# Performance work log

Hardware: AMD Instinct MI355X
Metric: run time of the kernel (lower is better)

The kernel has to match this reference:

```python
import jax, jax.numpy as jnp
import numpy as np
import math

B, S, D = 4, 2048, 1024
TAU = 0.5

def setup_inputs() -> dict:
    key = jax.random.key(0)
    ks = jax.random.split(key, 10)
    s = 1.0 / math.sqrt(D)
    return {
        "node_emb": jax.random.normal(ks[0], (B, S, D), jnp.float32),
        "label_emb": jax.random.normal(ks[1], (B, S, D), jnp.float32),
        "Wq": jax.random.uniform(ks[2], (D, D), jnp.float32, -s, s),
        "bq": jax.random.uniform(ks[3], (D,), jnp.float32, -s, s),
        "Wk": jax.random.uniform(ks[4], (D, D), jnp.float32, -s, s),
        "bk": jax.random.uniform(ks[5], (D,), jnp.float32, -s, s),
        "Wv": jax.random.uniform(ks[6], (D, D), jnp.float32, -s, s),
        "bv": jax.random.uniform(ks[7], (D,), jnp.float32, -s, s),
        "Wp": jax.random.uniform(ks[8], (D, D), jnp.float32, -s, s),
        "bp": jax.random.uniform(ks[9], (D,), jnp.float32, -s, s),
    }

def reference(node_emb, label_emb, Wq, bq, Wk, bk, Wv, bv, Wp, bp):
    # Q from label_emb; K, V from node_emb (torch Linear: x @ W.T + b)
    Q = label_emb @ Wq.T + bq          # [B, S, D]
    K = node_emb @ Wk.T + bk           # [B, S, D]
    V = node_emb @ Wv.T + bv           # [B, S, D]
    d = node_emb.shape[-1]
    score = jnp.einsum('bqd,bkd->bqk', Q, K) / jnp.sqrt(jnp.float32(d))
    # causal (lower-triangular) mask, masked_fill(-1e9) BEFORE the tau scale
    causal = jnp.tril(jnp.ones((score.shape[-2], score.shape[-1]), bool))
    score = jnp.where(causal[None, :, :], score, jnp.float32(-1e9))
    attn = jax.nn.softmax(score * TAU, axis=-1)  # [B, S, S]
    # proj_drop is Dropout(0.1); reference runs in eval mode (identity)
    z = jnp.einsum('bqk,bkd->bqd', attn, V)
    return z @ Wp.T + bp
```

## Files before the change

### kernel.cpp

```cpp
#include <hip/hip_runtime.h>
#include <hip/hip_bf16.h>
#include <stdint.h>

using bf16 = __hip_bfloat16;
typedef __bf16 bf16x8 __attribute__((ext_vector_type(8)));
typedef float f32x4 __attribute__((ext_vector_type(4)));
typedef unsigned short u16x8 __attribute__((ext_vector_type(8)));
typedef unsigned short u16x4 __attribute__((ext_vector_type(4)));

#define AS1 __attribute__((address_space(1)))
#define AS3 __attribute__((address_space(3)))

__device__ inline unsigned short f2b(float f) {
    union { __hip_bfloat16 h; unsigned short u; } cv;
    cv.h = __float2bfloat16(f);
    return cv.u;
}

__global__ __launch_bounds__(256) void cvt6(
    const float* __restrict__ i0, const float* __restrict__ i1,
    const float* __restrict__ i2, const float* __restrict__ i3,
    const float* __restrict__ i4, const float* __restrict__ i5,
    u16x8* __restrict__ o0, u16x8* __restrict__ o1,
    u16x8* __restrict__ o2, u16x8* __restrict__ o3,
    u16x8* __restrict__ o4, u16x8* __restrict__ o5,
    long nbig, long nsmall)
{
    const int y = blockIdx.y;
    const float* in = y == 0 ? i0 : (y == 1 ? i1 : (y == 2 ? i2 : (y == 3 ? i3 : (y == 4 ? i4 : i5))));
    u16x8* out = y == 0 ? o0 : (y == 1 ? o1 : (y == 2 ? o2 : (y == 3 ? o3 : (y == 4 ? o4 : o5))));
    const long n8 = (y < 2) ? nbig : nsmall;
    long i = (long)blockIdx.x * blockDim.x + threadIdx.x;
    const long stride = (long)gridDim.x * blockDim.x;
    const float4* in4 = (const float4*)in;
    for (; i < n8; i += stride) {
        float4 x = in4[2 * i], z = in4[2 * i + 1];
        u16x8 o;
        o[0] = f2b(x.x); o[1] = f2b(x.y); o[2] = f2b(x.z); o[3] = f2b(x.w);
        o[4] = f2b(z.x); o[5] = f2b(z.y); o[6] = f2b(z.z); o[7] = f2b(z.w);
        out[i] = o;
    }
}

template <typename T> __device__ inline void storev(T* p, float v);
template <> __device__ inline void storev<float>(float* p, float v) { *p = v; }
template <> __device__ inline void storev<bf16>(bf16* p, float v) { *p = __float2bfloat16(v); }

template <typename OutT, int MODE, int BN>
__global__ __launch_bounds__(512, 2) void gemmX(
    const bf16* __restrict__ A0, const bf16* __restrict__ A1,
    const bf16* __restrict__ B0p, const bf16* __restrict__ B1p,
    OutT* __restrict__ C0, OutT* __restrict__ C1,
    const float* __restrict__ bias0, const float* __restrict__ bias1,
    float scale, int lda, int ldb, int ldc, int Kdim,
    long sA, long sB, long sC)
{
    constexpr int LDSZ = (BN == 256) ? 131072 : ((MODE == 3) ? 99328 : 98304);
    constexpr int BUFS = (BN == 256) ? 65536 : 49152;
    __shared__ __align__(16) char lds[LDSZ];

    const int nwg = gridDim.x;
    const int bid = blockIdx.x;
    const int s = (nwg & 7) ? bid : ((bid & 7) * (nwg >> 3) + (bid >> 3));

    int bm, ccol0, rowB0, seg = 0, bn_s = 0, zidx = 0;
    const bf16 *A, *B;
    OutT* C;
    const float* bias = nullptr;

    if constexpr (MODE == 0) {
        bm = s >> 3; const int bnl = s & 7; seg = bnl >> 2;
        A = A0; B = B0p; rowB0 = bnl * 256;
        C = seg ? C1 : C0; bias = seg ? bias1 : bias0;
        ccol0 = (bnl & 3) * 256;
    } else if constexpr (MODE == 1) {
        seg = s >> 7; const int r = s & 127; bm = r >> 2; const int bn = r & 3;
        A = seg ? A1 : A0; B = seg ? B1p : B0p;
        C = seg ? C1 : C0; bias = seg ? nullptr : bias0;
        rowB0 = bn * 256; ccol0 = bn * 256;
    } else if constexpr (MODE == 2) {
        const int z = s / 36, f = s % 36;
        int m = 0;
        while ((m + 1) * (m + 2) / 2 <= f) ++m;
        bm = m; const int bn = f - m * (m + 1) / 2;
        bn_s = bn; zidx = z;
        A = A0 + (long)z * sA; B = B0p + (long)z * sB; C = C0 + (long)z * sC;
        rowB0 = bn * 256; ccol0 = bn * 256;
    } else {
        const int z = s >> 6, r = s & 63; bm = r >> 3; const int bn = r & 7;
        zidx = z;
        A = A0 + (long)z * sA; B = B0p + (long)z * sB; C = C0 + (long)z * sC;
        rowB0 = bn * 128; ccol0 = bn * 128; bias = bias0;
    }

    int KT = Kdim >> 6;
    if constexpr (MODE == 3) { const int lim = 4 * (bm + 1); if (lim < KT) KT = lim; }
    const int NIT = KT >> 1;

    const int tid = threadIdx.x;
    const int lane = tid & 63;
    const int w = tid >> 6;
    constexpr int WR = (BN == 256) ? 128 : 64;
    const int wm = (BN == 256) ? (w >> 2) : (w >> 1);
    const int wn = (BN == 256) ? (w & 3) : (w & 1);

    const int rowA0 = bm * 256;

    float* invl = (float*)(lds + 98304);
    if constexpr (MODE == 3) {
        if (tid < 256) {
            const float* part = (const float*)B1p + (((long)zidx * 8 + bm) * 32) * 256 + tid;
            float sum = 0.f;
            const int n4 = 4 * (bm + 1);
            for (int b4 = 0; b4 < n4; ++b4) sum += part[(long)b4 * 256];
            invl[tid] = 1.0f / sum;
        }
        asm volatile("s_waitcnt lgkmcnt(0)" ::: "memory");
        __builtin_amdgcn_sched_barrier(0);
    }

    const int rr  = tid >> 3;
    const int lch = (tid & 7) ^ (rr & 7);
    const bf16* gAt = A + (long)(rowA0 + rr) * lda + lch * 8;
    const bf16* gBt = B + (long)(rowB0 + rr) * ldb + lch * 8;

#define LA(b) (lds + (b) * BUFS)
#define LB(b) (lds + 32768 + (b) * BUFS)

    auto SG2 = [&](const bf16* g, int ld, char* dst) {
        __builtin_amdgcn_global_load_lds((const AS1 void*)g,
            (AS3 void*)(dst + tid * 16), 16, 0, 0);
        __builtin_amdgcn_global_load_lds((const AS1 void*)(g + (long)64 * ld),
            (AS3 void*)(dst + 8192 + tid * 16), 16, 0, 0);
    };
    auto ST_A = [&](int kt, int half, int b) {
        SG2(gAt + (long)kt * 64 + (long)half * 128 * lda, lda, LA(b) + half * 16384);
    };
    auto ST_B = [&](int kt, int half, int b) {
        SG2(gBt + (long)kt * 64 + (long)half * 128 * ldb, ldb, LB(b) + half * 16384);
    };
    auto ST_B1 = [&](int kt, int b) {
        SG2(gBt + (long)kt * 64, ldb, LB(b));
    };

    const int abase = (wm * WR + (lane & 15)) * 128;
    const int bbase = (wn * 64 + (lane & 15)) * 128;
    const int cc0 = (((lane >> 4) << 4)) ^ ((lane & 7) << 4);
    const int cc1 = cc0 ^ 64;

#define RAF(b, mh, mi, kk) (*(const bf16x8*)(LA(b) + abase + (mh)*8192 + (mi)*2048 + ((kk) ? cc1 : cc0)))
#define RBF(b, ni, kk)     (*(const bf16x8*)(LB(b) + bbase + (ni)*2048 + ((kk) ? cc1 : cc0)))

    f32x4 acc[(BN == 256) ? 8 : 4][4] = {};
    bf16x8 ar[4][2], blo[2][2], bhi[2][2];

#define RD_A2(b, mh, MI0) { ar[MI0][0] = RAF(b, mh, MI0, 0); ar[MI0][1] = RAF(b, mh, MI0, 1); \
                            ar[(MI0)+1][0] = RAF(b, mh, (MI0)+1, 0); ar[(MI0)+1][1] = RAF(b, mh, (MI0)+1, 1); }
#define RD_BLO(b)   { blo[0][0] = RBF(b, 0, 0); blo[0][1] = RBF(b, 0, 1); blo[1][0] = RBF(b, 1, 0); blo[1][1] = RBF(b, 1, 1); }
#define RD_BHI(b)   { bhi[0][0] = RBF(b, 2, 0); bhi[0][1] = RBF(b, 2, 1); bhi[1][0] = RBF(b, 3, 0); bhi[1][1] = RBF(b, 3, 1); }

#define MQ1(MI, bb, MH, NB) { \
    f32x4 t0_ = acc[(MH)*4 + (MI)][(NB)]; \
    t0_ = __builtin_amdgcn_mfma_f32_16x16x32_bf16(ar[MI][0], bb[0][0], t0_, 0, 0, 0); \
    t0_ = __builtin_amdgcn_mfma_f32_16x16x32_bf16(ar[MI][1], bb[0][1], t0_, 0, 0, 0); \
    acc[(MH)*4 + (MI)][(NB)] = t0_; \
    f32x4 t1_ = acc[(MH)*4 + (MI)][(NB) + 1]; \
    t1_ = __builtin_amdgcn_mfma_f32_16x16x32_bf16(ar[MI][0], bb[1][0], t1_, 0, 0, 0); \
    t1_ = __builtin_amdgcn_mfma_f32_16x16x32_bf16(ar[MI][1], bb[1][1], t1_, 0, 0, 0); \
    acc[(MH)*4 + (MI)][(NB) + 1] = t1_; }

#define WAIT_LGKM0 { asm volatile("s_waitcnt lgkmcnt(0)" ::: "memory"); __builtin_amdgcn_sched_barrier(0); }
#define WAIT_LGKM4 { asm volatile("s_waitcnt lgkmcnt(4)" ::: "memory"); __builtin_amdgcn_sched_barrier(0); }
#define SCHEDB     __builtin_amdgcn_sched_barrier(0)
#define PRE_SYNC { asm volatile("s_waitcnt lgkmcnt(0)" ::: "memory"); __builtin_amdgcn_sched_barrier(0); \
                   __builtin_amdgcn_s_barrier(); __builtin_amdgcn_sched_barrier(0); }

    auto BAR = [&]() { __builtin_amdgcn_s_barrier(); SCHEDB; };
    auto PRIO1 = [&]() { __builtin_amdgcn_s_setprio(1); };
    auto PRIO0 = [&]() { __builtin_amdgcn_s_setprio(0); };

    if constexpr (BN == 256) {
        ST_A(0, 0, 0); ST_A(0, 1, 0); ST_B(0, 0, 0); ST_B(0, 1, 0);
        ST_B(1, 0, 1); ST_B(1, 1, 1);
        asm volatile("s_waitcnt vmcnt(4)" ::: "memory");
        BAR();
        RD_BLO(0); RD_A2(0, 0, 0); RD_A2(0, 0, 2);

        for (int i = 0; i < NIT; ++i) {
            const int t0 = 2 * i;
            const bool last = (i == NIT - 1);

            ST_A(t0 + 1, 0, 1);
            PRE_SYNC; PRIO1();
            RD_BHI(0);
            MQ1(0, blo, 0, 0); MQ1(1, blo, 0, 0); MQ1(2, blo, 0, 0); MQ1(3, blo, 0, 0);
            PRIO0();

            ST_A(t0 + 1, 1, 1);
            PRE_SYNC; PRIO1();
            MQ1(0, bhi, 0, 2); MQ1(1, bhi, 0, 2); MQ1(2, bhi, 0, 2); MQ1(3, bhi, 0, 2);
            RD_A2(0, 1, 0); RD_A2(0, 1, 2);
            PRIO0();

            if (!last) ST_B(t0 + 2, 0, 0);
            PRE_SYNC; PRIO1();
            MQ1(0, bhi, 1, 2); MQ1(1, bhi, 1, 2); MQ1(2, bhi, 1, 2); MQ1(3, bhi, 1, 2);
            PRIO0();

            if (!last) { ST_B(t0 + 2, 1, 0);
                         asm volatile("s_waitcnt vmcnt(4)" ::: "memory"); }
            else       { asm volatile("s_waitcnt vmcnt(0)" ::: "memory"); }
            PRE_SYNC; PRIO1();
            MQ1(0, blo, 1, 0); MQ1(1, blo, 1, 0); MQ1(2, blo, 1, 0); MQ1(3, blo, 1, 0);
            RD_BLO(1); RD_A2(1, 0, 0); RD_A2(1, 0, 2);
            PRIO0();

            if (!last) ST_A(t0 + 2, 0, 0);
            PRE_SYNC; PRIO1();
            RD_BHI(1);
            MQ1(0, blo, 0, 0); MQ1(1, blo, 0, 0); MQ1(2, blo, 0, 0); MQ1(3, blo, 0, 0);
            PRIO0();

            if (!last) ST_A(t0 + 2, 1, 0);
            PRE_SYNC; PRIO1();
            MQ1(0, bhi, 0, 2); MQ1(1, bhi, 0, 2); MQ1(2, bhi, 0, 2); MQ1(3, bhi, 0, 2);
            RD_A2(1, 1, 0); RD_A2(1, 1, 2);
            PRIO0();

            if (!last) ST_B(t0 + 3, 0, 1);
            PRE_SYNC; PRIO1();
            MQ1(0, bhi, 1, 2); MQ1(1, bhi, 1, 2); MQ1(2, bhi, 1, 2); MQ1(3, bhi, 1, 2);
            PRIO0();

            if (!last) { ST_B(t0 + 3, 1, 1);
                         asm volatile("s_waitcnt vmcnt(4)" ::: "memory"); }
            PRE_SYNC; PRIO1();
            MQ1(0, blo, 1, 0); MQ1(1, blo, 1, 0); MQ1(2, blo, 1, 0); MQ1(3, blo, 1, 0);
            if (!last) { RD_BLO(0); RD_A2(0, 0, 0); RD_A2(0, 0, 2); }
            PRIO0();
        }
    } else {
        ST_A(0, 0, 0); ST_A(0, 1, 0); ST_B1(0, 0);
        ST_A(1, 0, 1); ST_A(1, 1, 1); ST_B1(1, 1);
        asm volatile("s_waitcnt vmcnt(6)" ::: "memory");
        BAR();

        for (int i = 0; i < NIT; ++i) {
            const int t0 = 2 * i;
            const bool last = (i == NIT - 1);

            RD_BLO(0); RD_A2(0, 0, 0); RD_A2(0, 0, 2); SCHEDB; RD_BHI(0);
            BAR(); WAIT_LGKM4; PRIO1();
            MQ1(0, blo, 0, 0); MQ1(1, blo, 0, 0); MQ1(2, blo, 0, 0); MQ1(3, blo, 0, 0);
            PRIO0(); BAR();

            if (!last) { ST_A(t0 + 2, 0, 0); ST_A(t0 + 2, 1, 0);
                         asm volatile("s_waitcnt vmcnt(4)" ::: "memory"); }
            else       { asm volatile("s_waitcnt vmcnt(0)" ::: "memory"); }
            BAR(); WAIT_LGKM0; PRIO1();
            MQ1(0, bhi, 0, 2); MQ1(1, bhi, 0, 2); MQ1(2, bhi, 0, 2); MQ1(3, bhi, 0, 2);
            PRIO0(); BAR();

            RD_BLO(1); RD_A2(1, 0, 0); RD_A2(1, 0, 2); SCHEDB; RD_BHI(1);
            if (!last) ST_B1(t0 + 2, 0);
            BAR(); WAIT_LGKM4; PRIO1();
            MQ1(0, blo, 0, 0); MQ1(1, blo, 0, 0); MQ1(2, blo, 0, 0); MQ1(3, blo, 0, 0);
            PRIO0(); BAR();

            if (!last) { ST_A(t0 + 3, 0, 1); ST_A(t0 + 3, 1, 1); ST_B1(t0 + 3, 1);
                         asm volatile("s_waitcnt vmcnt(6)" ::: "memory"); }
            BAR(); WAIT_LGKM0; PRIO1();
            MQ1(0, bhi, 0, 2); MQ1(1, bhi, 0, 2); MQ1(2, bhi, 0, 2); MQ1(3, bhi, 0, 2);
            PRIO0(); BAR();
        }
    }

    if constexpr (BN == 256) {
        char* tw = lds + w * 16384;
        if constexpr (MODE == 2) {
            const int q = lane >> 4, t = lane & 15;
            const bool diag = (bm == bn_s);
#pragma unroll
            for (int mi = 0; mi < 8; ++mi)
#pragma unroll
                for (int ni = 0; ni < 4; ++ni)
#pragma unroll
                    for (int j = 0; j < 4; ++j) {
                        float e = __expf(acc[mi][ni][j] * scale);
                        if (diag) {
                            const int rl = wm * 128 + mi * 16 + q * 4 + j;
                            const int cl = wn * 64 + t + ni * 16;
                            if (cl > rl) e = 0.f;
                        }
                        e = __bfloat162float(__float2bfloat16(e));
                        acc[mi][ni][j] = e;
                    }
            float* part = (float*)C1 + ((((long)zidx * 8 + bm) * 32) + bn_s * 4 + wn) * 256;
#pragma unroll
            for (int mi = 0; mi < 8; ++mi) {
                float rs0 = acc[mi][0][0] + acc[mi][1][0] + acc[mi][2][0] + acc[mi][3][0];
                float rs1 = acc[mi][0][1] + acc[mi][1][1] + acc[mi][2][1] + acc[mi][3][1];
                float rs2 = acc[mi][0][2] + acc[mi][1][2] + acc[mi][2][2] + acc[mi][3][2];
                float rs3 = acc[mi][0][3] + acc[mi][1][3] + acc[mi][2][3] + acc[mi][3][3];
#pragma unroll
                for (int d = 1; d < 16; d <<= 1) {
                    rs0 += __shfl_xor(rs0, d); rs1 += __shfl_xor(rs1, d);
                    rs2 += __shfl_xor(rs2, d); rs3 += __shfl_xor(rs3, d);
                }
                if (t == mi) {
                    float4 o; o.x = rs0; o.y = rs1; o.z = rs2; o.w = rs3;
                    *(float4*)(part + wm * 128 + mi * 16 + q * 4) = o;
                }
            }
        }
        if (MODE == 1 && seg == 1) {
#pragma unroll
            for (int ni = 0; ni < 4; ++ni) {
                const int cl = ni * 16 + (lane & 15);
                const int sw = 8 * (cl & 7);
#pragma unroll
                for (int mi = 0; mi < 8; ++mi) {
                    const int rlb = mi * 16 + ((lane >> 4) << 2);
                    u16x4 o;
                    o[0] = f2b(acc[mi][ni][0]); o[1] = f2b(acc[mi][ni][1]);
                    o[2] = f2b(acc[mi][ni][2]); o[3] = f2b(acc[mi][ni][3]);
                    *(u16x4*)(tw + cl * 256 + 2 * (rlb ^ sw)) = o;
                }
            }
            asm volatile("s_waitcnt lgkmcnt(0)" ::: "memory");
            __builtin_amdgcn_sched_barrier(0);
            const int m0 = rowA0 + wm * 128;
            const int z2 = m0 >> 11, mr = m0 & 2047;
            bf16* CT = (bf16*)C + (long)z2 * 2097152 + (long)(ccol0 + wn * 64 + lane) * 2048 + mr;
            const char* tr = tw + lane * 256;
            const int sw2 = lane & 7;
#pragma unroll
            for (int rb = 0; rb < 16; ++rb) {
                u16x8 v = *(const u16x8*)(tr + 16 * (rb ^ sw2));
                *(u16x8*)(CT + 8 * rb) = v;
            }
        } else {
            const float sc2 = (MODE == 2) ? 1.0f : scale;
            const int q = lane >> 4, t = lane & 15;
            const int c0 = ccol0 + wn * 64 + t;
#pragma unroll
            for (int mi = 0; mi < 8; ++mi) {
                char* tm = tw + mi * 2048;
#pragma unroll
                for (int ni = 0; ni < 4; ++ni) {
                    const float bv = bias ? bias[c0 + ni * 16] : 0.0f;
                    const int cb = (t + 16 * ni) * 2;
#pragma unroll
                    for (int j = 0; j < 4; ++j) {
                        const int rl = q * 4 + j;
                        *(bf16*)(tm + rl * 128 + (cb ^ ((rl & 7) << 4))) =
                            __float2bfloat16(acc[mi][ni][j] * sc2 + bv);
                    }
                }
            }
            asm volatile("s_waitcnt lgkmcnt(0)" ::: "memory");
            __builtin_amdgcn_sched_barrier(0);
            const int rr2 = lane >> 2, chb = (lane & 3) * 2;
            const int gr0 = rowA0 + wm * 128;
            bf16* Cb = (bf16*)C;
            const int gcb = ccol0 + wn * 64;
#pragma unroll
            for (int mi = 0; mi < 8; ++mi) {
                const char* tm = tw + mi * 2048;
                const long gr = gr0 + mi * 16 + rr2;
#pragma unroll
                for (int k = 0; k < 2; ++k) {
                    const int chunk = chb + k;
                    u16x8 v = *(const u16x8*)(tm + rr2 * 128 + ((chunk << 4) ^ ((rr2 & 7) << 4)));
                    *(u16x8*)(Cb + gr * (long)ldc + gcb + chunk * 8) = v;
                }
            }
        }
    } else {
        const int q = lane >> 4;
        const int r0 = rowA0 + wm * WR + (q << 2);
        const int rl0 = wm * WR + (q << 2);
        const int c0 = ccol0 + wn * 64 + (lane & 15);
#pragma unroll
        for (int mi = 0; mi < 4; ++mi) {
#pragma unroll
            for (int j = 0; j < 4; ++j) {
                const int rl = rl0 + mi * 16 + j;
                const float iv = (MODE == 3) ? invl[rl] : scale;
                const long r = r0 + mi * 16 + j;
#pragma unroll
                for (int ni = 0; ni < 4; ++ni) {
                    const int c = c0 + ni * 16;
                    const float bv = bias ? bias[c] : 0.0f;
                    storev<OutT>(&C[r * (long)ldc + c], acc[mi][ni][j] * iv + bv);
                }
            }
        }
    }
#undef RAF
#undef RBF
#undef RD_A2
#undef RD_BLO
#undef RD_BHI
#undef MQ1
#undef LA
#undef LB
}

extern "C" void kernel_launch(void* const* d_in, const int* in_sizes, int n_in,
                              void* d_out, int out_size, void* d_ws, size_t ws_size,
                              hipStream_t stream) {
    const int B = 4, S = 2048, D = 1024;
    const long MD = (long)B * S * D;
    const float scale = 0.5f / 32.0f;

    const float* node  = (const float*)d_in[0];
    const float* label = (const float*)d_in[1];
    const float* Wq = (const float*)d_in[2];
    const float* bq = (const float*)d_in[3];
    const float* Wk = (const float*)d_in[4];
    const float* bk = (const float*)d_in[5];
    const float* Wv = (const float*)d_in[6];
    const float* bv = (const float*)d_in[7];
    const float* Wp = (const float*)d_in[8];
    const float* bp = (const float*)d_in[9];
    float* out = (float*)d_out;

    char* ws = (char*)d_ws;
    bf16* nodeb  = (bf16*)(ws);
    bf16* VTb    = nodeb;
    bf16* labelb = (bf16*)(ws + 16777216);
    bf16* Wqb = (bf16*)(ws + 33554432);
    bf16* Wkb = (bf16*)(ws + 35651584);
    bf16* Wvb = (bf16*)(ws + 37748736);
    bf16* Wpb = (bf16*)(ws + 39845888);
    bf16* Qb  = (bf16*)(ws + 41943040);
    bf16* Kb  = (bf16*)(ws + 58720256);
    bf16* Vb  = (bf16*)(ws + 75497472);
    float* partial = (float*)(ws + 75497472);
    bf16* SP  = (bf16*)(ws + 92274688);
    if (ws_size < 125829120UL) return;

    cvt6<<<dim3(512, 6), 256, 0, stream>>>(
        node, label, Wq, Wk, Wv, Wp,
        (u16x8*)nodeb, (u16x8*)labelb, (u16x8*)Wqb, (u16x8*)Wkb, (u16x8*)Wvb, (u16x8*)Wpb,
        MD / 8, (long)D * D / 8);

    gemmX<bf16, 0, 256><<<256, 512, 0, stream>>>(
        nodeb, nullptr, Wkb, nullptr, Kb, Vb, bk, bv,
        1.0f, D, D, D, D, 0, 0, 0);

    gemmX<bf16, 1, 256><<<256, 512, 0, stream>>>(
        labelb, Vb, Wqb, Wpb, Qb, VTb, bq, nullptr,
        1.0f, D, D, D, D, 0, 0, 0);

    gemmX<bf16, 2, 256><<<144, 512, 0, stream>>>(
        Qb, nullptr, Kb, nullptr, SP, (bf16*)partial, nullptr, nullptr,
        scale, D, D, S, D, (long)S * D, (long)S * D, (long)S * S);

    gemmX<float, 3, 128><<<256, 512, 0, stream>>>(
        SP, nullptr, VTb, (const bf16*)partial, out, nullptr, bp, nullptr,
        1.0f, S, S, D, S, (long)S * S, (long)D * S, (long)S * D);
}
```

Baseline: 172.3 us.

## Replace causal PV GEMM with load-balanced kernel pairing row tiles

```diff
diff --git a/kernel.cpp b/kernel.cpp
--- a/kernel.cpp
+++ b/kernel.cpp
@@ -46,7 +46,7 @@
 template <> __device__ inline void storev<float>(float* p, float v) { *p = v; }
 template <> __device__ inline void storev<bf16>(bf16* p, float v) { *p = __float2bfloat16(v); }
 
-template <typename OutT, int MODE, int BN>
+template <typename OutT, int MODE>
 __global__ __launch_bounds__(512, 2) void gemmX(
     const bf16* __restrict__ A0, const bf16* __restrict__ A1,
     const bf16* __restrict__ B0p, const bf16* __restrict__ B1p,
@@ -55,9 +55,7 @@
     float scale, int lda, int ldb, int ldc, int Kdim,
     long sA, long sB, long sC)
 {
-    constexpr int LDSZ = (BN == 256) ? 131072 : ((MODE == 3) ? 99328 : 98304);
-    constexpr int BUFS = (BN == 256) ? 65536 : 49152;
-    __shared__ __align__(16) char lds[LDSZ];
+    __shared__ __align__(16) char lds[131072];
 
     const int nwg = gridDim.x;
     const int bid = blockIdx.x;
@@ -78,7 +76,7 @@
         A = seg ? A1 : A0; B = seg ? B1p : B0p;
         C = seg ? C1 : C0; bias = seg ? nullptr : bias0;
         rowB0 = bn * 256; ccol0 = bn * 256;
-    } else if constexpr (MODE == 2) {
+    } else {
         const int z = s / 36, f = s % 36;
         int m = 0;
         while ((m + 1) * (m + 2) / 2 <= f) ++m;
@@ -86,46 +84,26 @@
         bn_s = bn; zidx = z;
         A = A0 + (long)z * sA; B = B0p + (long)z * sB; C = C0 + (long)z * sC;
         rowB0 = bn * 256; ccol0 = bn * 256;
-    } else {
-        const int z = s >> 6, r = s & 63; bm = r >> 3; const int bn = r & 7;
-        zidx = z;
-        A = A0 + (long)z * sA; B = B0p + (long)z * sB; C = C0 + (long)z * sC;
-        rowB0 = bn * 128; ccol0 = bn * 128; bias = bias0;
     }
 
-    int KT = Kdim >> 6;
-    if constexpr (MODE == 3) { const int lim = 4 * (bm + 1); if (lim < KT) KT = lim; }
+    const int KT = Kdim >> 6;
     const int NIT = KT >> 1;
 
     const int tid = threadIdx.x;
     const int lane = tid & 63;
     const int w = tid >> 6;
-    constexpr int WR = (BN == 256) ? 128 : 64;
-    const int wm = (BN == 256) ? (w >> 2) : (w >> 1);
-    const int wn = (BN == 256) ? (w & 3) : (w & 1);
+    const int wm = w >> 2;
+    const int wn = w & 3;
 
     const int rowA0 = bm * 256;
-
-    float* invl = (float*)(lds + 98304);
-    if constexpr (MODE == 3) {
-        if (tid < 256) {
-            const float* part = (const float*)B1p + (((long)zidx * 8 + bm) * 32) * 256 + tid;
-            float sum = 0.f;
-            const int n4 = 4 * (bm + 1);
-            for (int b4 = 0; b4 < n4; ++b4) sum += part[(long)b4 * 256];
-            invl[tid] = 1.0f / sum;
-        }
-        asm volatile("s_waitcnt lgkmcnt(0)" ::: "memory");
-        __builtin_amdgcn_sched_barrier(0);
-    }
 
     const int rr  = tid >> 3;
     const int lch = (tid & 7) ^ (rr & 7);
     const bf16* gAt = A + (long)(rowA0 + rr) * lda + lch * 8;
     const bf16* gBt = B + (long)(rowB0 + rr) * ldb + lch * 8;
 
-#define LA(b) (lds + (b) * BUFS)
-#define LB(b) (lds + 32768 + (b) * BUFS)
+#define LA(b) (lds + (b) * 65536)
+#define LB(b) (lds + 32768 + (b) * 65536)
 
     auto SG2 = [&](const bf16* g, int ld, char* dst) {
         __builtin_amdgcn_global_load_lds((const AS1 void*)g,
@@ -139,11 +117,8 @@
     auto ST_B = [&](int kt, int half, int b) {
         SG2(gBt + (long)kt * 64 + (long)half * 128 * ldb, ldb, LB(b) + half * 16384);
     };
-    auto ST_B1 = [&](int kt, int b) {
-        SG2(gBt + (long)kt * 64, ldb, LB(b));
-    };
-
-    const int abase = (wm * WR + (lane & 15)) * 128;
+
+    const int abase = (wm * 128 + (lane & 15)) * 128;
     const int bbase = (wn * 64 + (lane & 15)) * 128;
     const int cc0 = (((lane >> 4) << 4)) ^ ((lane & 7) << 4);
     const int cc1 = cc0 ^ 64;
@@ -151,7 +126,7 @@
 #define RAF(b, mh, mi, kk) (*(const bf16x8*)(LA(b) + abase + (mh)*8192 + (mi)*2048 + ((kk) ? cc1 : cc0)))
 #define RBF(b, ni, kk)     (*(const bf16x8*)(LB(b) + bbase + (ni)*2048 + ((kk) ? cc1 : cc0)))
 
-    f32x4 acc[(BN == 256) ? 8 : 4][4] = {};
+    f32x4 acc[8][4] = {};
     bf16x8 ar[4][2], blo[2][2], bhi[2][2];
 
 #define RD_A2(b, mh, MI0) { ar[MI0][0] = RAF(b, mh, MI0, 0); ar[MI0][1] = RAF(b, mh, MI0, 1); \
@@ -169,8 +144,6 @@
     t1_ = __builtin_amdgcn_mfma_f32_16x16x32_bf16(ar[MI][1], bb[1][1], t1_, 0, 0, 0); \
     acc[(MH)*4 + (MI)][(NB) + 1] = t1_; }
 
-#define WAIT_LGKM0 { asm volatile("s_waitcnt lgkmcnt(0)" ::: "memory"); __builtin_amdgcn_sched_barrier(0); }
-#define WAIT_LGKM4 { asm volatile("s_waitcnt lgkmcnt(4)" ::: "memory"); __builtin_amdgcn_sched_barrier(0); }
 #define SCHEDB     __builtin_amdgcn_sched_barrier(0)
 #define PRE_SYNC { asm volatile("s_waitcnt lgkmcnt(0)" ::: "memory"); __builtin_amdgcn_sched_barrier(0); \
                    __builtin_amdgcn_s_barrier(); __builtin_amdgcn_sched_barrier(0); }
@@ -179,221 +152,163 @@
     auto PRIO1 = [&]() { __builtin_amdgcn_s_setprio(1); };
     auto PRIO0 = [&]() { __builtin_amdgcn_s_setprio(0); };
 
-    if constexpr (BN == 256) {
-        ST_A(0, 0, 0); ST_A(0, 1, 0); ST_B(0, 0, 0); ST_B(0, 1, 0);
-        ST_B(1, 0, 1); ST_B(1, 1, 1);
-        asm volatile("s_waitcnt vmcnt(4)" ::: "memory");
-        BAR();
-        RD_BLO(0); RD_A2(0, 0, 0); RD_A2(0, 0, 2);
-
-        for (int i = 0; i < NIT; ++i) {
-            const int t0 = 2 * i;
-            const bool last = (i == NIT - 1);
-
-            ST_A(t0 + 1, 0, 1);
-            PRE_SYNC; PRIO1();
-            RD_BHI(0);
-            MQ1(0, blo, 0, 0); MQ1(1, blo, 0, 0); MQ1(2, blo, 0, 0); MQ1(3, blo, 0, 0);
-            PRIO0();
-
-            ST_A(t0 + 1, 1, 1);
-            PRE_SYNC; PRIO1();
-            MQ1(0, bhi, 0, 2); MQ1(1, bhi, 0, 2); MQ1(2, bhi, 0, 2); MQ1(3, bhi, 0, 2);
-            RD_A2(0, 1, 0); RD_A2(0, 1, 2);
-            PRIO0();
-
-            if (!last) ST_B(t0 + 2, 0, 0);
-            PRE_SYNC; PRIO1();
-            MQ1(0, bhi, 1, 2); MQ1(1, bhi, 1, 2); MQ1(2, bhi, 1, 2); MQ1(3, bhi, 1, 2);
-            PRIO0();
-
-            if (!last) { ST_B(t0 + 2, 1, 0);
-                         asm volatile("s_waitcnt vmcnt(4)" ::: "memory"); }
-            else       { asm volatile("s_waitcnt vmcnt(0)" ::: "memory"); }
-            PRE_SYNC; PRIO1();
-            MQ1(0, blo, 1, 0); MQ1(1, blo, 1, 0); MQ1(2, blo, 1, 0); MQ1(3, blo, 1, 0);
-            RD_BLO(1); RD_A2(1, 0, 0); RD_A2(1, 0, 2);
-            PRIO0();
-
-            if (!last) ST_A(t0 + 2, 0, 0);
-            PRE_SYNC; PRIO1();
-            RD_BHI(1);
-            MQ1(0, blo, 0, 0); MQ1(1, blo, 0, 0); MQ1(2, blo, 0, 0); MQ1(3, blo, 0, 0);
-            PRIO0();
-
-            if (!last) ST_A(t0 + 2, 1, 0);
-            PRE_SYNC; PRIO1();
-            MQ1(0, bhi, 0, 2); MQ1(1, bhi, 0, 2); MQ1(2, bhi, 0, 2); MQ1(3, bhi, 0, 2);
-            RD_A2(1, 1, 0); RD_A2(1, 1, 2);
-            PRIO0();
-
-            if (!last) ST_B(t0 + 3, 0, 1);
-            PRE_SYNC; PRIO1();
-            MQ1(0, bhi, 1, 2); MQ1(1, bhi, 1, 2); MQ1(2, bhi, 1, 2); MQ1(3, bhi, 1, 2);
-            PRIO0();
-
-            if (!last) { ST_B(t0 + 3, 1, 1);
-                         asm volatile("s_waitcnt vmcnt(4)" ::: "memory"); }
-            PRE_SYNC; PRIO1();
-            MQ1(0, blo, 1, 0); MQ1(1, blo, 1, 0); MQ1(2, blo, 1, 0); MQ1(3, blo, 1, 0);
-            if (!last) { RD_BLO(0); RD_A2(0, 0, 0); RD_A2(0, 0, 2); }
-            PRIO0();
+    ST_A(0, 0, 0); ST_A(0, 1, 0); ST_B(0, 0, 0); ST_B(0, 1, 0);
+    ST_B(1, 0, 1); ST_B(1, 1, 1);
+    asm volatile("s_waitcnt vmcnt(4)" ::: "memory");
+    BAR();
+    RD_BLO(0); RD_A2(0, 0, 0); RD_A2(0, 0, 2);
+
+    for (int i = 0; i < NIT; ++i) {
+        const int t0 = 2 * i;
+        const bool last = (i == NIT - 1);
+
+        ST_A(t0 + 1, 0, 1);
+        PRE_SYNC; PRIO1();
+        RD_BHI(0);
+        MQ1(0, blo, 0, 0); MQ1(1, blo, 0, 0); MQ1(2, blo, 0, 0); MQ1(3, blo, 0, 0);
+        PRIO0();
+
+        ST_A(t0 + 1, 1, 1);
+        PRE_SYNC; PRIO1();
+        MQ1(0, bhi, 0, 2); MQ1(1, bhi, 0, 2); MQ1(2, bhi, 0, 2); MQ1(3, bhi, 0, 2);
+        RD_A2(0, 1, 0); RD_A2(0, 1, 2);
+        PRIO0();
+
+        if (!last) ST_B(t0 + 2, 0, 0);
+        PRE_SYNC; PRIO1();
+        MQ1(0, bhi, 1, 2); MQ1(1, bhi, 1, 2); MQ1(2, bhi, 1, 2); MQ1(3, bhi, 1, 2);
+        PRIO0();
+
+        if (!last) { ST_B(t0 + 2, 1, 0);
+                     asm volatile("s_waitcnt vmcnt(4)" ::: "memory"); }
+        else       { asm volatile("s_waitcnt vmcnt(0)" ::: "memory"); }
+        PRE_SYNC; PRIO1();
+        MQ1(0, blo, 1, 0); MQ1(1, blo, 1, 0); MQ1(2, blo, 1, 0); MQ1(3, blo, 1, 0);
+        RD_BLO(1); RD_A2(1, 0, 0); RD_A2(1, 0, 2);
+        PRIO0();
+
+        if (!last) ST_A(t0 + 2, 0, 0);
+        PRE_SYNC; PRIO1();
+        RD_BHI(1);
+        MQ1(0, blo, 0, 0); MQ1(1, blo, 0, 0); MQ1(2, blo, 0, 0); MQ1(3, blo, 0, 0);
+        PRIO0();
+
+        if (!last) ST_A(t0 + 2, 1, 0);
+        PRE_SYNC; PRIO1();
+        MQ1(0, bhi, 0, 2); MQ1(1, bhi, 0, 2); MQ1(2, bhi, 0, 2); MQ1(3, bhi, 0, 2);
+        RD_A2(1, 1, 0); RD_A2(1, 1, 2);
+        PRIO0();
+
+        if (!last) ST_B(t0 + 3, 0, 1);
+        PRE_SYNC; PRIO1();
+        MQ1(0, bhi, 1, 2); MQ1(1, bhi, 1, 2); MQ1(2, bhi, 1, 2); MQ1(3, bhi, 1, 2);
+        PRIO0();
+
+        if (!last) { ST_B(t0 + 3, 1, 1);
+                     asm volatile("s_waitcnt vmcnt(4)" ::: "memory"); }
+        PRE_SYNC; PRIO1();
+        MQ1(0, blo, 1, 0); MQ1(1, blo, 1, 0); MQ1(2, blo, 1, 0); MQ1(3, blo, 1, 0);
+        if (!last) { RD_BLO(0); RD_A2(0, 0, 0); RD_A2(0, 0, 2); }
+        PRIO0();
+    }
+
+    char* tw = lds + w * 16384;
+    if constexpr (MODE == 2) {
+        const int q = lane >> 4, t = lane & 15;
+        const bool diag = (bm == bn_s);
+#pragma unroll
+        for (int mi = 0; mi < 8; ++mi)
+#pragma unroll
+            for (int ni = 0; ni < 4; ++ni)
+#pragma unroll
+                for (int j = 0; j < 4; ++j) {
+                    float e = __expf(acc[mi][ni][j] * scale);
+                    if (diag) {
+                        const int rl = wm * 128 + mi * 16 + q * 4 + j;
+                        const int cl = wn * 64 + t + ni * 16;
+                        if (cl > rl) e = 0.f;
+                    }
+                    e = __bfloat162float(__float2bfloat16(e));
+                    acc[mi][ni][j] = e;
+                }
+        float* part = (float*)C1 + ((((long)zidx * 8 + bm) * 32) + bn_s * 4 + wn) * 256;
+#pragma unroll
+        for (int mi = 0; mi < 8; ++mi) {
+            float rs0 = acc[mi][0][0] + acc[mi][1][0] + acc[mi][2][0] + acc[mi][3][0];
+            float rs1 = acc[mi][0][1] + acc[mi][1][1] + acc[mi][2][1] + acc[mi][3][1];
+            float rs2 = acc[mi][0][2] + acc[mi][1][2] + acc[mi][2][2] + acc[mi][3][2];
+            float rs3 = acc[mi][0][3] + acc[mi][1][3] + acc[mi][2][3] + acc[mi][3][3];
+#pragma unroll
+            for (int d = 1; d < 16; d <<= 1) {
+                rs0 += __shfl_xor(rs0, d); rs1 += __shfl_xor(rs1, d);
+                rs2 += __shfl_xor(rs2, d); rs3 += __shfl_xor(rs3, d);
+            }
+            if (t == mi) {
+                float4 o; o.x = rs0; o.y = rs1; o.z = rs2; o.w = rs3;
+                *(float4*)(part + wm * 128 + mi * 16 + q * 4) = o;
+            }
+        }
+    }
+    if (MODE == 1 && seg == 1) {
+#pragma unroll
+        for (int ni = 0; ni < 4; ++ni) {
+            const int cl = ni * 16 + (lane & 15);
+            const int sw = 8 * (cl & 7);
+#pragma unroll
+            for (int mi = 0; mi < 8; ++mi) {
+                const int rlb = mi * 16 + ((lane >> 4) << 2);
+                u16x4 o;
+                o[0] = f2b(acc[mi][ni][0]); o[1] = f2b(acc[mi][ni][1]);
+                o[2] = f2b(acc[mi][ni][2]); o[3] = f2b(acc[mi][ni][3]);
+                *(u16x4*)(tw + cl * 256 + 2 * (rlb ^ sw)) = o;
+            }
+        }
+        asm volatile("s_waitcnt lgkmcnt(0)" ::: "memory");
+        __builtin_amdgcn_sched_barrier(0);
+        const int m0 = rowA0 + wm * 128;
+        const int z2 = m0 >> 11, mr = m0 & 2047;
+        bf16* CT = (bf16*)C + (long)z2 * 2097152 + (long)(ccol0 + wn * 64 + lane) * 2048 + mr;
+        const char* tr = tw + lane * 256;
+        const int sw2 = lane & 7;
+#pragma unroll
+        for (int rb = 0; rb < 16; ++rb) {
+            u16x8 v = *(const u16x8*)(tr + 16 * (rb ^ sw2));
+            *(u16x8*)(CT + 8 * rb) = v;
         }
     } else {
-        ST_A(0, 0, 0); ST_A(0, 1, 0); ST_B1(0, 0);
-        ST_A(1, 0, 1); ST_A(1, 1, 1); ST_B1(1, 1);
-        asm volatile("s_waitcnt vmcnt(6)" ::: "memory");
-        BAR();
-
-        for (int i = 0; i < NIT; ++i) {
-            const int t0 = 2 * i;
-            const bool last = (i == NIT - 1);
-
-            RD_BLO(0); RD_A2(0, 0, 0); RD_A2(0, 0, 2); SCHEDB; RD_BHI(0);
-            BAR(); WAIT_LGKM4; PRIO1();
-            MQ1(0, blo, 0, 0); MQ1(1, blo, 0, 0); MQ1(2, blo, 0, 0); MQ1(3, blo, 0, 0);
-            PRIO0(); BAR();
-
-            if (!last) { ST_A(t0 + 2, 0, 0); ST_A(t0 + 2, 1, 0);
-                         asm volatile("s_waitcnt vmcnt(4)" ::: "memory"); }
-            else       { asm volatile("s_waitcnt vmcnt(0)" ::: "memory"); }
-            BAR(); WAIT_LGKM0; PRIO1();
-            MQ1(0, bhi, 0, 2); MQ1(1, bhi, 0, 2); MQ1(2, bhi, 0, 2); MQ1(3, bhi, 0, 2);
-            PRIO0(); BAR();
-
-            RD_BLO(1); RD_A2(1, 0, 0); RD_A2(1, 0, 2); SCHEDB; RD_BHI(1);
-            if (!last) ST_B1(t0 + 2, 0);
-            BAR(); WAIT_LGKM4; PRIO1();
-            MQ1(0, blo, 0, 0); MQ1(1, blo, 0, 0); MQ1(2, blo, 0, 0); MQ1(3, blo, 0, 0);
-            PRIO0(); BAR();
-
-            if (!last) { ST_A(t0 + 3, 0, 1); ST_A(t0 + 3, 1, 1); ST_B1(t0 + 3, 1);
-                         asm volatile("s_waitcnt vmcnt(6)" ::: "memory"); }
-            BAR(); WAIT_LGKM0; PRIO1();
-            MQ1(0, bhi, 0, 2); MQ1(1, bhi, 0, 2); MQ1(2, bhi, 0, 2); MQ1(3, bhi, 0, 2);
-            PRIO0(); BAR();
-        }
-    }
-
-    if constexpr (BN == 256) {
-        char* tw = lds + w * 16384;
-        if constexpr (MODE == 2) {
-            const int q = lane >> 4, t = lane & 15;
-            const bool diag = (bm == bn_s);
-#pragma unroll
-            for (int mi = 0; mi < 8; ++mi)
-#pragma unroll
-                for (int ni = 0; ni < 4; ++ni)
-#pragma unroll
-                    for (int j = 0; j < 4; ++j) {
-                        float e = __expf(acc[mi][ni][j] * scale);
-                        if (diag) {
-                            const int rl = wm * 128 + mi * 16 + q * 4 + j;
-                            const int cl = wn * 64 + t + ni * 16;
-                            if (cl > rl) e = 0.f;
-                        }
-                        e = __bfloat162float(__float2bfloat16(e));
-                        acc[mi][ni][j] = e;
-                    }
-            float* part = (float*)C1 + ((((long)zidx * 8 + bm) * 32) + bn_s * 4 + wn) * 256;
-#pragma unroll
-            for (int mi = 0; mi < 8; ++mi) {
-                float rs0 = acc[mi][0][0] + acc[mi][1][0] + acc[mi][2][0] + acc[mi][3][0];
-                float rs1 = acc[mi][0][1] + acc[mi][1][1] + acc[mi][2][1] + acc[mi][3][1];
-                float rs2 = acc[mi][0][2] + acc[mi][1][2] + acc[mi][2][2] + acc[mi][3][2];
-                float rs3 = acc[mi][0][3] + acc[mi][1][3] + acc[mi][2][3] + acc[mi][3][3];
-#pragma unroll
-                for (int d = 1; d < 16; d <<= 1) {
-                    rs0 += __shfl_xor(rs0, d); rs1 += __shfl_xor(rs1, d);
-                    rs2 += __shfl_xor(rs2, d); rs3 += __shfl_xor(rs3, d);
+        const float sc2 = (MODE == 2) ? 1.0f : scale;
+        const int q = lane >> 4, t = lane & 15;
+        const int c0 = ccol0 + wn * 64 + t;
+#pragma unroll
+        for (int mi = 0; mi < 8; ++mi) {
+            char* tm = tw + mi * 2048;
+#pragma unroll
+            for (int ni = 0; ni < 4; ++ni) {
+                const float bv = bias ? bias[c0 + ni * 16] : 0.0f;
+                const int cb = (t + 16 * ni) * 2;
+#pragma unroll
+                for (int j = 0; j < 4; ++j) {
+                    const int rl = q * 4 + j;
+                    *(bf16*)(tm + rl * 128 + (cb ^ ((rl & 7) << 4))) =
+                        __float2bfloat16(acc[mi][ni][j] * sc2 + bv);
                 }
-                if (t == mi) {
-                    float4 o; o.x = rs0; o.y = rs1; o.z = rs2; o.w = rs3;
-                    *(float4*)(part + wm * 128 + mi * 16 + q * 4) = o;
-                }
-            }
-        }
-        if (MODE == 1 && seg == 1) {
-#pragma unroll
-            for (int ni = 0; ni < 4; ++ni) {
-                const int cl = ni * 16 + (lane & 15);
-                const int sw = 8 * (cl & 7);
-#pragma unroll
-                for (int mi = 0; mi < 8; ++mi) {
-                    const int rlb = mi * 16 + ((lane >> 4) << 2);
-                    u16x4 o;
-                    o[0] = f2b(acc[mi][ni][0]); o[1] = f2b(acc[mi][ni][1]);
-                    o[2] = f2b(acc[mi][ni][2]); o[3] = f2b(acc[mi][ni][3]);
-                    *(u16x4*)(tw + cl * 256 + 2 * (rlb ^ sw)) = o;
-                }
-            }
-            asm volatile("s_waitcnt lgkmcnt(0)" ::: "memory");
-            __builtin_amdgcn_sched_barrier(0);
-            const int m0 = rowA0 + wm * 128;
-            const int z2 = m0 >> 11, mr = m0 & 2047;
-            bf16* CT = (bf16*)C + (long)z2 * 2097152 + (long)(ccol0 + wn * 64 + lane) * 2048 + mr;
-            const char* tr = tw + lane * 256;
-            const int sw2 = lane & 7;
-#pragma unroll
-            for (int rb = 0; rb < 16; ++rb) {
-                u16x8 v = *(const u16x8*)(tr + 16 * (rb ^ sw2));
-                *(u16x8*)(CT + 8 * rb) = v;
-            }
-        } else {
-            const float sc2 = (MODE == 2) ? 1.0f : scale;
-            const int q = lane >> 4, t = lane & 15;
-            const int c0 = ccol0 + wn * 64 + t;
-#pragma unroll
-            for (int mi = 0; mi < 8; ++mi) {
-                char* tm = tw + mi * 2048;
-#pragma unroll
-                for (int ni = 0; ni < 4; ++ni) {
-                    const float bv = bias ? bias[c0 + ni * 16] : 0.0f;
-                    const int cb = (t + 16 * ni) * 2;
-#pragma unroll
-                    for (int j = 0; j < 4; ++j) {
-                        const int rl = q * 4 + j;
-                        *(bf16*)(tm + rl * 128 + (cb ^ ((rl & 7) << 4))) =
-                            __float2bfloat16(acc[mi][ni][j] * sc2 + bv);
-                    }
-                }
-            }
-            asm volatile("s_waitcnt lgkmcnt(0)" ::: "memory");
-            __builtin_amdgcn_sched_barrier(0);
-            const int rr2 = lane >> 2, chb = (lane & 3) * 2;
-            const int gr0 = rowA0 + wm * 128;
-            bf16* Cb = (bf16*)C;
-            const int gcb = ccol0 + wn * 64;
-#pragma unroll
-            for (int mi = 0; mi < 8; ++mi) {
-                const char* tm = tw + mi * 2048;
-                const long gr = gr0 + mi * 16 + rr2;
-#pragma unroll
-                for (int k = 0; k < 2; ++k) {
-                    const int chunk = chb + k;
-                    u16x8 v = *(const u16x8*)(tm + rr2 * 128 + ((chunk << 4) ^ ((rr2 & 7) << 4)));
-                    *(u16x8*)(Cb + gr * (long)ldc + gcb + chunk * 8) = v;
-                }
-            }
-        }
-    } else {
-        const int q = lane >> 4;
-        const int r0 = rowA0 + wm * WR + (q << 2);
-        const int rl0 = wm * WR + (q << 2);
-        const int c0 = ccol0 + wn * 64 + (lane & 15);
-#pragma unroll
-        for (int mi = 0; mi < 4; ++mi) {
-#pragma unroll
-            for (int j = 0; j < 4; ++j) {
-                const int rl = rl0 + mi * 16 + j;
-                const float iv = (MODE == 3) ? invl[rl] : scale;
-                const long r = r0 + mi * 16 + j;
-#pragma unroll
-                for (int ni = 0; ni < 4; ++ni) {
-                    const int c = c0 + ni * 16;
-                    const float bv = bias ? bias[c] : 0.0f;
-                    storev<OutT>(&C[r * (long)ldc + c], acc[mi][ni][j] * iv + bv);
-                }
+            }
+        }
+        asm volatile("s_waitcnt lgkmcnt(0)" ::: "memory");
+        __builtin_amdgcn_sched_barrier(0);
+        const int rr2 = lane >> 2, chb = (lane & 3) * 2;
+        const int gr0 = rowA0 + wm * 128;
+        bf16* Cb = (bf16*)C;
+        const int gcb = ccol0 + wn * 64;
+#pragma unroll
+        for (int mi = 0; mi < 8; ++mi) {
+            const char* tm = tw + mi * 2048;
+            const long gr = gr0 + mi * 16 + rr2;
+#pragma unroll
+            for (int k = 0; k < 2; ++k) {
+                const int chunk = chb + k;
+                u16x8 v = *(const u16x8*)(tm + rr2 * 128 + ((chunk << 4) ^ ((rr2 & 7) << 4)));
+                *(u16x8*)(Cb + gr * (long)ldc + gcb + chunk * 8) = v;
             }
         }
     }
@@ -405,6 +320,156 @@
 #undef MQ1
 #undef LA
 #undef LB
+}
+
+__global__ __launch_bounds__(512, 2) void pv_bal(
+    const bf16* __restrict__ P, const bf16* __restrict__ VT,
+    const float* __restrict__ part, float* __restrict__ out,
+    const float* __restrict__ bias)
+{
+    __shared__ __align__(16) char lds[99328];
+    float* invl = (float*)(lds + 98304);
+
+    const int nwg = gridDim.x;
+    const int bid = blockIdx.x;
+    const int s = (bid & 7) * (nwg >> 3) + (bid >> 3);
+    const int z = s >> 6, r = s & 63;
+    const int pr = r >> 3, bn = r & 7;
+    const int bmA = pr, bmB = 15 - pr;
+
+    const bf16* Pz = P + (long)z * 2048 * 2048;
+    const bf16* Vz = VT + (long)z * 1024 * 2048;
+
+    const int tid = threadIdx.x;
+    const int lane = tid & 63;
+    const int w = tid >> 6;
+    const int wm = w >> 2, wn = w & 3;
+    const int rr = tid >> 3;
+    const int lch = (tid & 7) ^ (rr & 7);
+
+    if (tid < 256) {
+        const int half = tid >> 7, rloc = tid & 127;
+        const int grow = (half ? bmB : bmA) * 128 + rloc;
+        const int b256 = grow >> 8, rin = grow & 255;
+        const float* pp = part + (((long)z * 8 + b256) * 32) * 256 + rin;
+        const int n4 = 4 * (b256 + 1);
+        float s0 = 0.f, s1 = 0.f, s2 = 0.f, s3 = 0.f;
+        int b4 = 0;
+        for (; b4 + 4 <= n4; b4 += 4) {
+            s0 += pp[(long)b4 * 256];       s1 += pp[(long)(b4 + 1) * 256];
+            s2 += pp[(long)(b4 + 2) * 256]; s3 += pp[(long)(b4 + 3) * 256];
+        }
+        for (; b4 < n4; ++b4) s0 += pp[(long)b4 * 256];
+        invl[tid] = 1.0f / ((s0 + s1) + (s2 + s3));
+    }
+
+    const bf16* gBt = Vz + (long)(bn * 128 + rr) * 2048 + lch * 8;
+    const bf16* gAtA = Pz + (long)(bmA * 128 + rr) * 2048 + lch * 8;
+    const bf16* gAtB = Pz + (long)(bmB * 128 + rr) * 2048 + lch * 8;
+
+    auto SG2 = [&](const bf16* g, char* dst) {
+        __builtin_amdgcn_global_load_lds((const AS1 void*)g,
+            (AS3 void*)(dst + tid * 16), 16, 0, 0);
+        __builtin_amdgcn_global_load_lds((const AS1 void*)(g + (long)64 * 2048),
+            (AS3 void*)(dst + 8192 + tid * 16), 16, 0, 0);
+    };
+    auto ST = [&](const bf16* gAt, int kt, int b) {
+        SG2(gAt + (long)kt * 64, lds + b * 32768);
+        SG2(gBt + (long)kt * 64, lds + b * 32768 + 16384);
+    };
+
+    const int abase0 = (wm * 64 + (lane & 15)) * 128;
+    const int bbase0 = 16384 + (wn * 32 + (lane & 15)) * 128;
+    const int cc0 = ((lane >> 4) << 4) ^ ((lane & 7) << 4);
+    const int cc1 = cc0 ^ 64;
+
+    f32x4 acc[4][2];
+    bf16x8 ar[4][2], br[2][2];
+
+    auto RDF = [&](int t) {
+        const char* base = lds + (t % 3) * 32768;
+#pragma unroll
+        for (int mi = 0; mi < 4; ++mi) {
+            ar[mi][0] = *(const bf16x8*)(base + abase0 + mi * 2048 + cc0);
+            ar[mi][1] = *(const bf16x8*)(base + abase0 + mi * 2048 + cc1);
+        }
+#pragma unroll
+        for (int ni = 0; ni < 2; ++ni) {
+            br[ni][0] = *(const bf16x8*)(base + bbase0 + ni * 2048 + cc0);
+            br[ni][1] = *(const bf16x8*)(base + bbase0 + ni * 2048 + cc1);
+        }
+    };
+    auto MFMA16 = [&]() {
+#pragma unroll
+        for (int mi = 0; mi < 4; ++mi)
+#pragma unroll
+            for (int ni = 0; ni < 2; ++ni) {
+                f32x4 t_ = acc[mi][ni];
+                t_ = __builtin_amdgcn_mfma_f32_16x16x32_bf16(ar[mi][0], br[ni][0], t_, 0, 0, 0);
+                t_ = __builtin_amdgcn_mfma_f32_16x16x32_bf16(ar[mi][1], br[ni][1], t_, 0, 0, 0);
+                acc[mi][ni] = t_;
+            }
+    };
+    auto ZERO = [&]() {
+#pragma unroll
+        for (int mi = 0; mi < 4; ++mi)
+#pragma unroll
+            for (int ni = 0; ni < 2; ++ni) acc[mi][ni] = f32x4{0.f, 0.f, 0.f, 0.f};
+    };
+    auto tile_pass = [&](const bf16* gAt, int KT) {
+        RDF(0);
+        for (int t = 0; t < KT; ++t) {
+            if (t + 2 < KT) {
+                ST(gAt, t + 2, (t + 2) % 3);
+                asm volatile("s_waitcnt vmcnt(4)" ::: "memory");
+            } else if (t + 1 < KT) {
+                asm volatile("s_waitcnt vmcnt(0)" ::: "memory");
+            }
+            asm volatile("s_waitcnt lgkmcnt(0)" ::: "memory");
+            __builtin_amdgcn_sched_barrier(0);
+            __builtin_amdgcn_s_barrier();
+            __builtin_amdgcn_sched_barrier(0);
+            __builtin_amdgcn_s_setprio(1);
+            MFMA16();
+            if (t + 1 < KT) RDF(t + 1);
+            __builtin_amdgcn_s_setprio(0);
+        }
+    };
+    auto epi = [&](int bm, int invoff) {
+        const int q = lane >> 4, t16 = lane & 15;
+        const int c0 = bn * 128 + wn * 32 + t16;
+        float* op = out + ((long)z * 2048 + (long)bm * 128) * 1024;
+#pragma unroll
+        for (int mi = 0; mi < 4; ++mi)
+#pragma unroll
+            for (int j = 0; j < 4; ++j) {
+                const int rl = wm * 64 + mi * 16 + q * 4 + j;
+                const float iv = invl[invoff + rl];
+#pragma unroll
+                for (int ni = 0; ni < 2; ++ni) {
+                    const int c = c0 + ni * 16;
+                    op[(long)rl * 1024 + c] = acc[mi][ni][j] * iv + bias[c];
+                }
+            }
+    };
+
+    const int KTA = 2 * (bmA + 1), KTB = 2 * (bmB + 1);
+
+    ST(gAtA, 0, 0); ST(gAtA, 1, 1);
+    asm volatile("s_waitcnt vmcnt(4)" ::: "memory");
+    __builtin_amdgcn_s_barrier();
+    __builtin_amdgcn_sched_barrier(0);
+    ZERO();
+    tile_pass(gAtA, KTA);
+
+    ST(gAtB, 0, 0); ST(gAtB, 1, 1);
+    epi(bmA, 0);
+    asm volatile("s_waitcnt vmcnt(0)" ::: "memory");
+    __builtin_amdgcn_s_barrier();
+    __builtin_amdgcn_sched_barrier(0);
+    ZERO();
+    tile_pass(gAtB, KTB);
+    epi(bmB, 128);
 }
 
 extern "C" void kernel_launch(void* const* d_in, const int* in_sizes, int n_in,
@@ -446,19 +511,17 @@
         (u16x8*)nodeb, (u16x8*)labelb, (u16x8*)Wqb, (u16x8*)Wkb, (u16x8*)Wvb, (u16x8*)Wpb,
         MD / 8, (long)D * D / 8);
 
-    gemmX<bf16, 0, 256><<<256, 512, 0, stream>>>(
+    gemmX<bf16, 0><<<256, 512, 0, stream>>>(
         nodeb, nullptr, Wkb, nullptr, Kb, Vb, bk, bv,
         1.0f, D, D, D, D, 0, 0, 0);
 
-    gemmX<bf16, 1, 256><<<256, 512, 0, stream>>>(
+    gemmX<bf16, 1><<<256, 512, 0, stream>>>(
         labelb, Vb, Wqb, Wpb, Qb, VTb, bq, nullptr,
         1.0f, D, D, D, D, 0, 0, 0);
 
-    gemmX<bf16, 2, 256><<<144, 512, 0, stream>>>(
-        Qb, nullptr, Kb, nullptr, SP, (bf16*)partial, nullptr, nullptr,
+    gemmX<bf16, 2><<<144, 512, 0, stream>>>(
+        Qb, nullptr, Kb, (bf16*)nullptr, SP, (bf16*)partial, nullptr, nullptr,
         scale, D, D, S, D, (long)S * D, (long)S * D, (long)S * S);
 
-    gemmX<float, 3, 128><<<256, 512, 0, stream>>>(
-        SP, nullptr, VTb, (const bf16*)partial, out, nullptr, bp, nullptr,
-        1.0f, S, S, D, S, (long)S * S, (long)D * S, (long)S * D);
+    pv_bal<<<256, 512, 0, stream>>>(SP, VTb, partial, out, bp);
 }
```

New measurement: 153.4 us. 1.12x faster.
